# Kernel optimization log

Hardware: AMD Instinct MI355X
Metric: run time of the kernel (lower is better)

Reference implementation:

```python
import jax, jax.numpy as jnp
import numpy as np

H, DH = 8, 64          # num_heads, head_dim
DM = H * DH            # hidden_dim = 512
LAM = 1.0              # lambda_param
SCALE = 1.0 / np.sqrt(DH)


def setup_inputs() -> dict:
    key = jax.random.key(0)
    ks = jax.random.split(key, 12)
    B, N, R = 2, 2048, 16
    s = DM ** -0.5
    inp = {
        "x": jax.random.normal(ks[0], (B, N, DM), jnp.float32),
        "pde_residuals": jax.random.normal(ks[1], (B, N, R), jnp.float32),
        "mask": jnp.ones((B, 1, N, N), jnp.int32),
        "Wq": jax.random.normal(ks[2], (DM, DM), jnp.float32) * s,
        "bq": jax.random.normal(ks[3], (DM,), jnp.float32) * 0.01,
        "Wk": jax.random.normal(ks[4], (DM, DM), jnp.float32) * s,
        "bk": jax.random.normal(ks[5], (DM,), jnp.float32) * 0.01,
        "Wv": jax.random.normal(ks[6], (DM, DM), jnp.float32) * s,
        "bv": jax.random.normal(ks[7], (DM,), jnp.float32) * 0.01,
        "Wo": jax.random.normal(ks[8], (DM, DM), jnp.float32) * s,
        "bo": jax.random.normal(ks[9], (DM,), jnp.float32) * 0.01,
    }
    return inp


def reference(x, pde_residuals, mask, Wq, bq, Wk, bk, Wv, bv, Wo, bo):
    B, N, _ = x.shape
    # torch nn.Linear: y = x @ W.T + b
    q = (x @ Wq.T + bq).reshape(B, N, H, DH)
    k = (x @ Wk.T + bk).reshape(B, N, H, DH)
    v = (x @ Wv.T + bv).reshape(B, N, H, DH)
    # [B,H,N,N]
    scores = jnp.einsum('bqhd,bkhd->bhqk', q, k) * SCALE
    # residual bias: rb.unsqueeze(1) - rb.unsqueeze(2) -> bias[b,i,j] = rb[b,j] - rb[b,i]
    rb = jnp.linalg.norm(pde_residuals, axis=-1)            # [B,N]
    bias = rb[:, None, None, :] - rb[:, None, :, None]       # [B,1,N,N]
    scores = scores - LAM * bias
    scores = jnp.where(mask == 0, -jnp.inf, scores)
    attn = jax.nn.softmax(scores, axis=-1)                   # dropout is identity in eval
    out = jnp.einsum('bhqk,bkhd->bqhd', attn, v).reshape(B, N, DM)
    return out @ Wo.T + bo
```

## Files before the change

kernel.cpp:

```cpp
#include <hip/hip_runtime.h>
#include <hip/hip_bf16.h>
#include <math.h>

#define B_ 2
#define N_ 2048
#define H_ 8
#define DH_ 64
#define DM_ 512
#define R_ 16
#define LAM_ 1.0f
#define SCALE_ 0.125f
#define LOG2E_ 1.44269504088896f
#define QSCALE_ (SCALE_ * LOG2E_)
#define DEFER_THR_ 11.5415603f

typedef unsigned short u16;
typedef unsigned int u32;
typedef u16 u16x4 __attribute__((ext_vector_type(4)));
typedef u16 u16x8 __attribute__((ext_vector_type(8)));
typedef __bf16 bf16x8 __attribute__((ext_vector_type(8)));
typedef float f32x4 __attribute__((ext_vector_type(4)));

#define EXP2(x) __builtin_amdgcn_exp2f(x)

static __device__ __forceinline__ u16 f2bf(float f) {
    union { float f; unsigned u; } v; v.f = f;
    unsigned r = v.u + 0x7FFF + ((v.u >> 16) & 1);
    return (u16)(r >> 16);
}

static __device__ __forceinline__ u32 pack_bf16(float lo, float hi) {
    float2 f2; f2.x = lo; f2.y = hi;
    __hip_bfloat162 h2 = __float22bfloat162_rn(f2);
    u32 r;
    __builtin_memcpy(&r, &h2, 4);
    return r;
}

static __device__ __forceinline__ void gl_lds16(const void* g, void* l) {
    __builtin_amdgcn_global_load_lds(
        (const __attribute__((address_space(1))) unsigned*)g,
        (__attribute__((address_space(3))) unsigned*)l, 16, 0, 0);
}

__global__ __launch_bounds__(256) void prep(
    const float* __restrict__ x, const float* __restrict__ wq,
    const float* __restrict__ wk, const float* __restrict__ wv,
    const float* __restrict__ wo, u16* __restrict__ xb, u16* __restrict__ wqb,
    u16* __restrict__ wkb, u16* __restrict__ wvb, u16* __restrict__ wob) {
    int y = blockIdx.y;
    const float* src; u16* dst; int n;
    switch (y) {
        case 0: src = x;  dst = xb;  n = 2097152; break;
        case 1: src = wq; dst = wqb; n = 262144;  break;
        case 2: src = wk; dst = wkb; n = 262144;  break;
        case 3: src = wv; dst = wvb; n = 262144;  break;
        default: src = wo; dst = wob; n = 262144; break;
    }
    int i = (blockIdx.x * 256 + threadIdx.x) * 8;
    if (i >= n) return;
    float4 a = *(const float4*)(src + i);
    float4 b = *(const float4*)(src + i + 4);
    u16x8 o;
    o[0] = f2bf(a.x); o[1] = f2bf(a.y); o[2] = f2bf(a.z); o[3] = f2bf(a.w);
    o[4] = f2bf(b.x); o[5] = f2bf(b.y); o[6] = f2bf(b.z); o[7] = f2bf(b.w);
    *(u16x8*)(dst + i) = o;
}

struct Acc { f32x4 v[2][2]; };

static __device__ __forceinline__ Acc gemm_core(const u16* __restrict__ A,
                                                const u16* __restrict__ W,
                                                int m0, int nn0, char* LDSB) {
    int t = threadIdx.x, l = t & 63, w = t >> 6;
    int lg = l >> 4, li = l & 15;
    int wr = w >> 1, wc = w & 1;
    Acc acc;
#pragma unroll
    for (int m = 0; m < 2; ++m)
#pragma unroll
        for (int n = 0; n < 2; ++n) acc.v[m][n] = (f32x4){0.f, 0.f, 0.f, 0.f};

    int srl = l >> 3;
    int colb = ((l & 7) * 16) ^ (srl << 4);

    for (int k0 = 0; k0 < DM_; k0 += 64) {
        __syncthreads();
#pragma unroll
        for (int i = 0; i < 2; ++i) {
            int c = w * 2 + i;
            int row = c * 8 + srl;
            gl_lds16(A + (size_t)(m0 + row) * DM_ + k0 + (colb >> 1),
                     LDSB + c * 1024);
            gl_lds16(W + (size_t)(nn0 + row) * DM_ + k0 + (colb >> 1),
                     LDSB + 8192 + c * 1024);
        }
        __syncthreads();
#pragma unroll
        for (int kk = 0; kk < 2; ++kk) {
            bf16x8 af[2], bfr[2];
#pragma unroll
            for (int m = 0; m < 2; ++m) {
                int r = wr * 32 + m * 16 + li;
                af[m] = *(const bf16x8*)(LDSB + r * 128 +
                                         ((kk * 64 + lg * 16) ^ ((r & 7) << 4)));
            }
#pragma unroll
            for (int n = 0; n < 2; ++n) {
                int r = wc * 32 + n * 16 + li;
                bfr[n] = *(const bf16x8*)(LDSB + 8192 + r * 128 +
                                          ((kk * 64 + lg * 16) ^ ((r & 7) << 4)));
            }
#pragma unroll
            for (int m = 0; m < 2; ++m)
#pragma unroll
                for (int n = 0; n < 2; ++n)
                    acc.v[m][n] = __builtin_amdgcn_mfma_f32_16x16x32_bf16(
                        af[m], bfr[n], acc.v[m][n], 0, 0, 0);
        }
    }
    return acc;
}

struct Acc2 { f32x4 v[4][2]; };

static __device__ __forceinline__ Acc2 gemm_core2(const u16* __restrict__ A,
                                                  const u16* __restrict__ W,
                                                  int m0, int nn0, char* LDSB) {
    int t = threadIdx.x, l = t & 63, w = t >> 6;
    int lg = l >> 4, li = l & 15;
    int wr = w >> 1, wc = w & 1;
    Acc2 acc;
#pragma unroll
    for (int m = 0; m < 4; ++m)
#pragma unroll
        for (int n = 0; n < 2; ++n) acc.v[m][n] = (f32x4){0.f, 0.f, 0.f, 0.f};

    int srl = l >> 3;
    int colb = ((l & 7) * 16) ^ (srl << 4);

    for (int k0 = 0; k0 < DM_; k0 += 64) {
        __syncthreads();
#pragma unroll
        for (int i = 0; i < 4; ++i) {
            int c = w * 4 + i;
            int row = c * 8 + srl;
            gl_lds16(A + (size_t)(m0 + row) * DM_ + k0 + (colb >> 1),
                     LDSB + c * 1024);
        }
#pragma unroll
        for (int i = 0; i < 2; ++i) {
            int c = w * 2 + i;
            int row = c * 8 + srl;
            gl_lds16(W + (size_t)(nn0 + row) * DM_ + k0 + (colb >> 1),
                     LDSB + 16384 + c * 1024);
        }
        __syncthreads();
#pragma unroll
        for (int kk = 0; kk < 2; ++kk) {
            bf16x8 af[4], bfr[2];
#pragma unroll
            for (int m = 0; m < 4; ++m) {
                int r = wr * 64 + m * 16 + li;
                af[m] = *(const bf16x8*)(LDSB + r * 128 +
                                         ((kk * 64 + lg * 16) ^ ((r & 7) << 4)));
            }
#pragma unroll
            for (int n = 0; n < 2; ++n) {
                int r = wc * 32 + n * 16 + li;
                bfr[n] = *(const bf16x8*)(LDSB + 16384 + r * 128 +
                                          ((kk * 64 + lg * 16) ^ ((r & 7) << 4)));
            }
#pragma unroll
            for (int m = 0; m < 4; ++m)
#pragma unroll
                for (int n = 0; n < 2; ++n)
                    acc.v[m][n] = __builtin_amdgcn_mfma_f32_16x16x32_bf16(
                        af[m], bfr[n], acc.v[m][n], 0, 0, 0);
        }
    }
    return acc;
}

__global__ __launch_bounds__(256) void qkv_fused(
    const u16* __restrict__ xb, const u16* __restrict__ wqb,
    const u16* __restrict__ wkb, const u16* __restrict__ wvb,
    const float* __restrict__ bq, const float* __restrict__ bk,
    const float* __restrict__ bv, const int* __restrict__ mask,
    const float* __restrict__ pde, u16* __restrict__ q_bf,
    u16* __restrict__ k_bf, u16* __restrict__ vt,
    float* __restrict__ rbs, int* __restrict__ flags) {
    __shared__ char LDSB[24576];
    int bid = blockIdx.x, t = threadIdx.x;

    if (bid < 768) {
        int y = bid >> 5;
        int which = y >> 3;
        int nn0 = (y & 7) * 64;
        const u16* W = which == 0 ? wqb : which == 1 ? wkb : wvb;
        const float* bias = which == 0 ? bq : which == 1 ? bk : bv;
        int m0 = (bid & 31) * 128;
        Acc2 acc = gemm_core2(xb, W, m0, nn0, LDSB);

        int l = t & 63, w = t >> 6;
        int lg = l >> 4, li = l & 15;
        int wr = w >> 1, wc = w & 1;
        float scale = which == 0 ? QSCALE_ : 1.0f;
#pragma unroll
        for (int n = 0; n < 2; ++n) {
            int col = nn0 + wc * 32 + n * 16 + li;
            float bv_ = bias[col];
            if (which < 2) {
                u16* dst = which == 0 ? q_bf : k_bf;
#pragma unroll
                for (int m = 0; m < 4; ++m)
#pragma unroll
                    for (int r = 0; r < 4; ++r) {
                        int row = m0 + wr * 64 + m * 16 + lg * 4 + r;
                        dst[(size_t)row * DM_ + col] =
                            f2bf((acc.v[m][n][r] + bv_) * scale);
                    }
            } else {
                int h = col >> 6, d = col & 63;
#pragma unroll
                for (int m = 0; m < 4; ++m) {
                    int row = m0 + wr * 64 + m * 16 + lg * 4;
                    int b = row >> 11, nb = row & (N_ - 1);
                    u16x4 o;
#pragma unroll
                    for (int r = 0; r < 4; ++r) o[r] = f2bf(acc.v[m][n][r] + bv_);
                    *(u16x4*)(vt + ((size_t)((b * 8 + h) * 64 + d)) * N_ + nb) = o;
                }
            }
        }
    } else if (bid < 2816) {
        int idx = bid - 768;
        int b = idx >> 10, qt = (idx >> 5) & 31, kt = idx & 31;
        int* red = (int*)LDSB;
        if (t == 0) *red = 0;
        __syncthreads();
        int any = 0;
        for (int c = t; c < 1024; c += 256) {
            int row = c >> 4, seg = c & 15;
            int4 m4 = *(const int4*)(mask + (size_t)b * N_ * N_ +
                                     (size_t)(qt * 64 + row) * N_ + kt * 64 + seg * 4);
            any |= (m4.x == 0) | (m4.y == 0) | (m4.z == 0) | (m4.w == 0);
        }
        if (__ballot(any)) {
            if ((t & 63) == 0) atomicOr(red, 1);
        }
        __syncthreads();
        if (t == 0) flags[(b * 32 + qt) * 32 + kt] = *red;
    } else {
        int i = (bid - 2816) * 256 + t;
        if (i >= B_ * N_) return;
        const float4* p = (const float4*)(pde + (size_t)i * R_);
        float s = 0.f;
#pragma unroll
        for (int j = 0; j < 4; ++j) {
            float4 v = p[j];
            s += v.x * v.x + v.y * v.y + v.z * v.z + v.w * v.w;
        }
        rbs[i] = LAM_ * LOG2E_ * sqrtf(s);
    }
}

__global__ __launch_bounds__(256) void gemm_out(
    const u16* __restrict__ aob, const u16* __restrict__ wob,
    const float* __restrict__ bo, float* __restrict__ out) {
    __shared__ char LDSB[24576];
    int nn0 = blockIdx.y * 64;
    int m0 = blockIdx.x * 64;
    Acc acc = gemm_core(aob, wob, m0, nn0, LDSB);

    int t = threadIdx.x, l = t & 63, w = t >> 6;
    int lg = l >> 4, li = l & 15;
    int wr = w >> 1, wc = w & 1;
#pragma unroll
    for (int n = 0; n < 2; ++n) {
        int col = nn0 + wc * 32 + n * 16 + li;
        float bv_ = bo[col];
#pragma unroll
        for (int m = 0; m < 2; ++m)
#pragma unroll
            for (int r = 0; r < 4; ++r) {
                int row = m0 + wr * 32 + m * 16 + lg * 4 + r;
                out[(size_t)row * DM_ + col] = acc.v[m][n][r] + bv_;
            }
    }
}

__global__ __launch_bounds__(512) void attn12(
    const u16* __restrict__ qb, const u16* __restrict__ kb,
    const u16* __restrict__ vtb, const float* __restrict__ rbs,
    const int* __restrict__ mask, const int* __restrict__ flags,
    u16* __restrict__ aob) {
    __shared__ char KVB[2][2][16384];
    __shared__ char PsB[8][2048];

    int t = threadIdx.x, l = t & 63, w = t >> 6;
    int g2 = w >> 2, wq = w & 3;
    int raw = blockIdx.x;
    int sid = (raw & 7) * 64 + (raw >> 3);
    int bh = sid >> 5, qg = sid & 31;
    int b = bh >> 3, h = bh & 7;
    int m0 = qg * 64 + wq * 16;
    int lg = l >> 4, li = l & 15;
    int k0base = g2 * 1024;

    int srl = l >> 3;
    int colb = ((l & 7) * 16) ^ (srl << 4);

    bf16x8 qa[2];
    {
        const u16* qrow = qb + (size_t)(b * N_ + m0 + li) * DM_ + h * DH_;
        qa[0] = __builtin_bit_cast(bf16x8, *(const u16x8*)(qrow + lg * 8));
        qa[1] = __builtin_bit_cast(bf16x8, *(const u16x8*)(qrow + 32 + lg * 8));
    }

    f32x4 o[4];
#pragma unroll
    for (int dt = 0; dt < 4; ++dt) o[dt] = (f32x4){0.f, 0.f, 0.f, 0.f};
    float mrun = -INFINITY, lrun = 0.f;

    auto STAGE = [&](int bufi, int k0s) {
        char* base = &KVB[g2][bufi][0];
#pragma unroll
        for (int c = 0; c < 2; ++c) {
            int chunk = wq * 2 + c;
            int row = chunk * 8 + srl;
            gl_lds16(kb + (size_t)(b * N_ + k0s + row) * DM_ + h * DH_ + (colb >> 1),
                     base + chunk * 1024);
            gl_lds16(vtb + ((size_t)(bh * DH_ + row)) * N_ + k0s + (colb >> 1),
                     base + 8192 + chunk * 1024);
        }
    };

    STAGE(0, k0base);
    __syncthreads();

    char* pwbase = &PsB[w][0] + li * 16 + ((lg & 1) << 3);
    int slot_lohi = (lg >> 1);

    int buf = 0;
    for (int tt = 0; tt < 16; ++tt) {
        int k0 = k0base + tt * 64;
        if (tt < 15) STAGE(buf ^ 1, k0 + 64);

        const char* Kb = &KVB[g2][buf][0];
        const char* Vb = &KVB[g2][buf][8192];
        int flag = flags[(b * 32 + qg) * 32 + (k0 >> 6)];

        f32x4 st[4];
        __builtin_amdgcn_s_setprio(1);
#pragma unroll
        for (int kt = 0; kt < 4; ++kt) {
            st[kt] = (f32x4){0.f, 0.f, 0.f, 0.f};
#pragma unroll
            for (int s = 0; s < 2; ++s) {
                int key = kt * 16 + li;
                bf16x8 kf = *(const bf16x8*)(Kb + key * 128 +
                                             ((s * 64 + lg * 16) ^ ((key & 7) << 4)));
                st[kt] = __builtin_amdgcn_mfma_f32_16x16x32_bf16(kf, qa[s], st[kt],
                                                                 0, 0, 0);
            }
        }
        __builtin_amdgcn_s_setprio(0);

#pragma unroll
        for (int kt = 0; kt < 4; ++kt) {
            float4 rb4 = *(const float4*)(rbs + b * N_ + k0 + kt * 16 + lg * 4);
            st[kt][0] -= rb4.x; st[kt][1] -= rb4.y;
            st[kt][2] -= rb4.z; st[kt][3] -= rb4.w;
        }
        if (flag) {
#pragma unroll
            for (int kt = 0; kt < 4; ++kt)
#pragma unroll
                for (int r = 0; r < 4; ++r) {
                    int rowg = m0 + li;
                    int keyg = k0 + kt * 16 + lg * 4 + r;
                    if (mask[(size_t)b * N_ * N_ + (size_t)rowg * N_ + keyg] == 0)
                        st[kt][r] = -INFINITY;
                }
        }

        float m0_ = fmaxf(fmaxf(st[0][0], st[0][1]), fmaxf(st[0][2], st[0][3]));
        float m1_ = fmaxf(fmaxf(st[1][0], st[1][1]), fmaxf(st[1][2], st[1][3]));
        float m2_ = fmaxf(fmaxf(st[2][0], st[2][1]), fmaxf(st[2][2], st[2][3]));
        float m3_ = fmaxf(fmaxf(st[3][0], st[3][1]), fmaxf(st[3][2], st[3][3]));
        float mymax = fmaxf(fmaxf(m0_, m1_), fmaxf(m2_, m3_));
        if (!__all(mymax - mrun <= DEFER_THR_)) {
            float pmax = mymax;
            pmax = fmaxf(pmax, __shfl_xor(pmax, 16));
            pmax = fmaxf(pmax, __shfl_xor(pmax, 32));
            float mnew = fmaxf(fmaxf(mrun, pmax), -3.0e38f);
            float corr = EXP2(mrun - mnew);
            mrun = mnew;
            lrun *= corr;
#pragma unroll
            for (int dt = 0; dt < 4; ++dt)
#pragma unroll
                for (int r = 0; r < 4; ++r) o[dt][r] *= corr;
        }

#pragma unroll
        for (int kt = 0; kt < 4; ++kt) {
            float p0 = EXP2(st[kt][0] - mrun);
            float p1 = EXP2(st[kt][1] - mrun);
            float p2 = EXP2(st[kt][2] - mrun);
            float p3 = EXP2(st[kt][3] - mrun);
            lrun += (p0 + p1) + (p2 + p3);
            uint2 pkw;
            pkw.x = pack_bf16(p0, p1);
            pkw.y = pack_bf16(p2, p3);
            int slot = (kt >> 1) * 4 + (kt & 1) * 2 + slot_lohi;
            *(uint2*)(pwbase + (slot << 8)) = pkw;
        }

        bf16x8 pf[2];
#pragma unroll
        for (int s = 0; s < 2; ++s)
            pf[s] = *(const bf16x8*)(&PsB[w][0] + ((s * 4 + lg) << 8) + li * 16);
        __builtin_amdgcn_s_setprio(1);
#pragma unroll
        for (int dt = 0; dt < 4; ++dt)
#pragma unroll
            for (int s = 0; s < 2; ++s) {
                int d = dt * 16 + li;
                bf16x8 vf = *(const bf16x8*)(Vb + d * 128 +
                                             ((s * 64 + lg * 16) ^ ((d & 7) << 4)));
                o[dt] = __builtin_amdgcn_mfma_f32_16x16x32_bf16(vf, pf[s], o[dt],
                                                                0, 0, 0);
            }
        __builtin_amdgcn_s_setprio(0);

        __syncthreads();
        buf ^= 1;
    }

    lrun += __shfl_xor(lrun, 16);
    lrun += __shfl_xor(lrun, 32);

    float* cmb = (float*)&KVB[0][0][0];
    float* mlc = (float*)&PsB[0][0];
    if (g2 == 1) {
        float* dst = cmb + wq * 1088;
#pragma unroll
        for (int dt = 0; dt < 4; ++dt)
            *(f32x4*)(dst + li * 68 + dt * 16 + lg * 4) = o[dt];
        if (lg == 0) {
            float2 ml; ml.x = mrun; ml.y = lrun;
            *(float2*)(mlc + (wq * 16 + li) * 2) = ml;
        }
    }
    __syncthreads();
    if (g2 == 0) {
        float2 ml1 = *(const float2*)(mlc + (wq * 16 + li) * 2);
        float m = fmaxf(mrun, ml1.x);
        float w0 = EXP2(mrun - m), w1 = EXP2(ml1.x - m);
        float denom = 1.f / (lrun * w0 + ml1.y * w1);
        w0 *= denom; w1 *= denom;
        const float* src = cmb + wq * 1088;
        u16* orow = aob + (size_t)(b * N_ + m0 + li) * DM_ + h * DH_;
#pragma unroll
        for (int dt = 0; dt < 4; ++dt) {
            f32x4 p1 = *(const f32x4*)(src + li * 68 + dt * 16 + lg * 4);
            u16x4 ov;
#pragma unroll
            for (int r = 0; r < 4; ++r)
                ov[r] = f2bf(o[dt][r] * w0 + p1[r] * w1);
            *(u16x4*)(orow + dt * 16 + lg * 4) = ov;
        }
    }
}

extern "C" void kernel_launch(void* const* d_in, const int* in_sizes, int n_in,
                              void* d_out, int out_size, void* d_ws, size_t ws_size,
                              hipStream_t stream) {
    const float* x   = (const float*)d_in[0];
    const float* pde = (const float*)d_in[1];
    const int*   msk = (const int*)d_in[2];
    const float* Wq  = (const float*)d_in[3];
    const float* bq  = (const float*)d_in[4];
    const float* Wk  = (const float*)d_in[5];
    const float* bk  = (const float*)d_in[6];
    const float* Wv  = (const float*)d_in[7];
    const float* bv  = (const float*)d_in[8];
    const float* Wo  = (const float*)d_in[9];
    const float* bo  = (const float*)d_in[10];
    float* out = (float*)d_out;

    const size_t MAT = (size_t)B_ * N_ * DM_;
    const size_t WSZ = (size_t)DM_ * DM_;
    u16* xb   = (u16*)d_ws;
    u16* q_bf = xb + MAT;
    u16* k_bf = q_bf + MAT;
    u16* vt   = k_bf + MAT;
    u16* aob  = vt + MAT;
    u16* wqb  = aob + MAT;
    u16* wkb  = wqb + WSZ;
    u16* wvb  = wkb + WSZ;
    u16* wob  = wvb + WSZ;
    float* rbs = (float*)(wob + WSZ);
    int* flags = (int*)(rbs + B_ * N_);

    prep<<<dim3(1024, 5), 256, 0, stream>>>(x, Wq, Wk, Wv, Wo,
                                            xb, wqb, wkb, wvb, wob);

    qkv_fused<<<2832, 256, 0, stream>>>(xb, wqb, wkb, wvb, bq, bk, bv,
                                        msk, pde, q_bf, k_bf, vt, rbs, flags);

    attn12<<<512, 512, 0, stream>>>(q_bf, k_bf, vt, rbs, msk, flags, aob);

    gemm_out<<<dim3(64, 8), 256, 0, stream>>>(aob, wob, bo, out);
}
```

Baseline: 67.69 us.

## Switch attention to 32x32x16 MFMA with 32-row query tiles per wave

Rewrites the attention kernel so each wave handles 32 query rows with 32x32x16 bf16 MFMAs instead of 16 rows with 16x16x32. The block drops from 8 to 4 waves, and each wave stages twice as many K/V chunks. The P tile layout is reworked into a swizzled per-row buffer. The goal is fewer LDS fragment reads per FLOP and better MFMA efficiency. The cost is higher register pressure from the 16-wide accumulators and less latency hiding with fewer waves per block.

```diff
diff --git a/kernel.cpp b/kernel.cpp
--- a/kernel.cpp
+++ b/kernel.cpp
@@ -20,6 +20,7 @@
 typedef u16 u16x8 __attribute__((ext_vector_type(8)));
 typedef __bf16 bf16x8 __attribute__((ext_vector_type(8)));
 typedef float f32x4 __attribute__((ext_vector_type(4)));
+typedef float f32x16 __attribute__((ext_vector_type(16)));
 
 #define EXP2(x) __builtin_amdgcn_exp2f(x)
 
@@ -290,44 +291,49 @@
     }
 }
 
-__global__ __launch_bounds__(512) void attn12(
+__global__ __launch_bounds__(256) void attn13(
     const u16* __restrict__ qb, const u16* __restrict__ kb,
     const u16* __restrict__ vtb, const float* __restrict__ rbs,
     const int* __restrict__ mask, const int* __restrict__ flags,
     u16* __restrict__ aob) {
     __shared__ char KVB[2][2][16384];
-    __shared__ char PsB[8][2048];
+    __shared__ char PsB[4][4096];
 
     int t = threadIdx.x, l = t & 63, w = t >> 6;
-    int g2 = w >> 2, wq = w & 3;
+    int qh = w >> 1, ks = w & 1;
     int raw = blockIdx.x;
     int sid = (raw & 7) * 64 + (raw >> 3);
     int bh = sid >> 5, qg = sid & 31;
     int b = bh >> 3, h = bh & 7;
-    int m0 = qg * 64 + wq * 16;
-    int lg = l >> 4, li = l & 15;
-    int k0base = g2 * 1024;
+    int m0 = qg * 64 + qh * 32;
+    int q5 = l & 31, hi = l >> 5;
+    int k0base = ks * 1024;
 
     int srl = l >> 3;
     int colb = ((l & 7) * 16) ^ (srl << 4);
-
-    bf16x8 qa[2];
+    int q7s = (q5 & 7) << 4;
+
+    bf16x8 qa[4];
     {
-        const u16* qrow = qb + (size_t)(b * N_ + m0 + li) * DM_ + h * DH_;
-        qa[0] = __builtin_bit_cast(bf16x8, *(const u16x8*)(qrow + lg * 8));
-        qa[1] = __builtin_bit_cast(bf16x8, *(const u16x8*)(qrow + 32 + lg * 8));
-    }
-
-    f32x4 o[4];
-#pragma unroll
-    for (int dt = 0; dt < 4; ++dt) o[dt] = (f32x4){0.f, 0.f, 0.f, 0.f};
+        const u16* qrow = qb + (size_t)(b * N_ + m0 + q5) * DM_ + h * DH_;
+#pragma unroll
+        for (int s = 0; s < 4; ++s)
+            qa[s] = __builtin_bit_cast(bf16x8,
+                        *(const u16x8*)(qrow + s * 16 + hi * 8));
+    }
+
+    f32x16 o[2];
+#pragma unroll
+    for (int db = 0; db < 2; ++db)
+#pragma unroll
+        for (int r = 0; r < 16; ++r) o[db][r] = 0.f;
     float mrun = -INFINITY, lrun = 0.f;
 
     auto STAGE = [&](int bufi, int k0s) {
-        char* base = &KVB[g2][bufi][0];
-#pragma unroll
-        for (int c = 0; c < 2; ++c) {
-            int chunk = wq * 2 + c;
+        char* base = &KVB[ks][bufi][0];
+#pragma unroll
+        for (int c = 0; c < 4; ++c) {
+            int chunk = qh * 4 + c;
             int row = chunk * 8 + srl;
             gl_lds16(kb + (size_t)(b * N_ + k0s + row) * DM_ + h * DH_ + (colb >> 1),
                      base + chunk * 1024);
@@ -339,139 +345,146 @@
     STAGE(0, k0base);
     __syncthreads();
 
-    char* pwbase = &PsB[w][0] + li * 16 + ((lg & 1) << 3);
-    int slot_lohi = (lg >> 1);
+    char* prow = &PsB[w][0] + q5 * 128;
 
     int buf = 0;
     for (int tt = 0; tt < 16; ++tt) {
         int k0 = k0base + tt * 64;
         if (tt < 15) STAGE(buf ^ 1, k0 + 64);
 
-        const char* Kb = &KVB[g2][buf][0];
-        const char* Vb = &KVB[g2][buf][8192];
+        const char* Kb = &KVB[ks][buf][0];
+        const char* Vb = &KVB[ks][buf][8192];
         int flag = flags[(b * 32 + qg) * 32 + (k0 >> 6)];
 
-        f32x4 st[4];
+        f32x16 st[2];
         __builtin_amdgcn_s_setprio(1);
 #pragma unroll
-        for (int kt = 0; kt < 4; ++kt) {
-            st[kt] = (f32x4){0.f, 0.f, 0.f, 0.f};
-#pragma unroll
-            for (int s = 0; s < 2; ++s) {
-                int key = kt * 16 + li;
-                bf16x8 kf = *(const bf16x8*)(Kb + key * 128 +
-                                             ((s * 64 + lg * 16) ^ ((key & 7) << 4)));
-                st[kt] = __builtin_amdgcn_mfma_f32_16x16x32_bf16(kf, qa[s], st[kt],
-                                                                 0, 0, 0);
+        for (int kb2 = 0; kb2 < 2; ++kb2) {
+#pragma unroll
+            for (int r = 0; r < 16; ++r) st[kb2][r] = 0.f;
+#pragma unroll
+            for (int s = 0; s < 4; ++s) {
+                bf16x8 kf = *(const bf16x8*)(Kb + (kb2 * 32 + q5) * 128 +
+                                             ((s * 32 + hi * 16) ^ q7s));
+                st[kb2] = __builtin_amdgcn_mfma_f32_32x32x16_bf16(
+                    kf, qa[s], st[kb2], 0, 0, 0);
             }
         }
         __builtin_amdgcn_s_setprio(0);
 
 #pragma unroll
-        for (int kt = 0; kt < 4; ++kt) {
-            float4 rb4 = *(const float4*)(rbs + b * N_ + k0 + kt * 16 + lg * 4);
-            st[kt][0] -= rb4.x; st[kt][1] -= rb4.y;
-            st[kt][2] -= rb4.z; st[kt][3] -= rb4.w;
-        }
+        for (int kb2 = 0; kb2 < 2; ++kb2)
+#pragma unroll
+            for (int g = 0; g < 4; ++g) {
+                float4 rb4 = *(const float4*)(rbs + b * N_ + k0 + kb2 * 32 +
+                                              8 * g + 4 * hi);
+                st[kb2][4 * g + 0] -= rb4.x;
+                st[kb2][4 * g + 1] -= rb4.y;
+                st[kb2][4 * g + 2] -= rb4.z;
+                st[kb2][4 * g + 3] -= rb4.w;
+            }
         if (flag) {
 #pragma unroll
-            for (int kt = 0; kt < 4; ++kt)
-#pragma unroll
-                for (int r = 0; r < 4; ++r) {
-                    int rowg = m0 + li;
-                    int keyg = k0 + kt * 16 + lg * 4 + r;
+            for (int kb2 = 0; kb2 < 2; ++kb2)
+#pragma unroll
+                for (int r = 0; r < 16; ++r) {
+                    int keyg = k0 + kb2 * 32 + (r & 3) + 8 * (r >> 2) + 4 * hi;
+                    int rowg = m0 + q5;
                     if (mask[(size_t)b * N_ * N_ + (size_t)rowg * N_ + keyg] == 0)
-                        st[kt][r] = -INFINITY;
+                        st[kb2][r] = -INFINITY;
                 }
         }
 
-        float m0_ = fmaxf(fmaxf(st[0][0], st[0][1]), fmaxf(st[0][2], st[0][3]));
-        float m1_ = fmaxf(fmaxf(st[1][0], st[1][1]), fmaxf(st[1][2], st[1][3]));
-        float m2_ = fmaxf(fmaxf(st[2][0], st[2][1]), fmaxf(st[2][2], st[2][3]));
-        float m3_ = fmaxf(fmaxf(st[3][0], st[3][1]), fmaxf(st[3][2], st[3][3]));
-        float mymax = fmaxf(fmaxf(m0_, m1_), fmaxf(m2_, m3_));
+        float mymax = -INFINITY;
+#pragma unroll
+        for (int kb2 = 0; kb2 < 2; ++kb2)
+#pragma unroll
+            for (int r = 0; r < 16; ++r) mymax = fmaxf(mymax, st[kb2][r]);
         if (!__all(mymax - mrun <= DEFER_THR_)) {
-            float pmax = mymax;
-            pmax = fmaxf(pmax, __shfl_xor(pmax, 16));
-            pmax = fmaxf(pmax, __shfl_xor(pmax, 32));
+            float pmax = fmaxf(mymax, __shfl_xor(mymax, 32));
             float mnew = fmaxf(fmaxf(mrun, pmax), -3.0e38f);
             float corr = EXP2(mrun - mnew);
             mrun = mnew;
             lrun *= corr;
 #pragma unroll
-            for (int dt = 0; dt < 4; ++dt)
-#pragma unroll
-                for (int r = 0; r < 4; ++r) o[dt][r] *= corr;
-        }
-
-#pragma unroll
-        for (int kt = 0; kt < 4; ++kt) {
-            float p0 = EXP2(st[kt][0] - mrun);
-            float p1 = EXP2(st[kt][1] - mrun);
-            float p2 = EXP2(st[kt][2] - mrun);
-            float p3 = EXP2(st[kt][3] - mrun);
-            lrun += (p0 + p1) + (p2 + p3);
-            uint2 pkw;
-            pkw.x = pack_bf16(p0, p1);
-            pkw.y = pack_bf16(p2, p3);
-            int slot = (kt >> 1) * 4 + (kt & 1) * 2 + slot_lohi;
-            *(uint2*)(pwbase + (slot << 8)) = pkw;
-        }
-
-        bf16x8 pf[2];
-#pragma unroll
-        for (int s = 0; s < 2; ++s)
-            pf[s] = *(const bf16x8*)(&PsB[w][0] + ((s * 4 + lg) << 8) + li * 16);
+            for (int db = 0; db < 2; ++db)
+#pragma unroll
+                for (int r = 0; r < 16; ++r) o[db][r] *= corr;
+        }
+
+#pragma unroll
+        for (int kb2 = 0; kb2 < 2; ++kb2)
+#pragma unroll
+            for (int g = 0; g < 4; ++g) {
+                float p0 = EXP2(st[kb2][4 * g + 0] - mrun);
+                float p1 = EXP2(st[kb2][4 * g + 1] - mrun);
+                float p2 = EXP2(st[kb2][4 * g + 2] - mrun);
+                float p3 = EXP2(st[kb2][4 * g + 3] - mrun);
+                lrun += (p0 + p1) + (p2 + p3);
+                uint2 pkw;
+                pkw.x = pack_bf16(p0, p1);
+                pkw.y = pack_bf16(p2, p3);
+                *(uint2*)(prow + ((kb2 * 64 + 16 * g + 8 * hi) ^ q7s)) = pkw;
+            }
+
         __builtin_amdgcn_s_setprio(1);
 #pragma unroll
-        for (int dt = 0; dt < 4; ++dt)
-#pragma unroll
-            for (int s = 0; s < 2; ++s) {
-                int d = dt * 16 + li;
-                bf16x8 vf = *(const bf16x8*)(Vb + d * 128 +
-                                             ((s * 64 + lg * 16) ^ ((d & 7) << 4)));
-                o[dt] = __builtin_amdgcn_mfma_f32_16x16x32_bf16(vf, pf[s], o[dt],
-                                                                0, 0, 0);
-            }
+        for (int ks16 = 0; ks16 < 4; ++ks16) {
+            bf16x8 pf = *(const bf16x8*)(prow + ((ks16 * 32 + hi * 16) ^ q7s));
+#pragma unroll
+            for (int db = 0; db < 2; ++db) {
+                bf16x8 vf = *(const bf16x8*)(Vb + (db * 32 + q5) * 128 +
+                                             ((ks16 * 32 + hi * 16) ^ q7s));
+                o[db] = __builtin_amdgcn_mfma_f32_32x32x16_bf16(
+                    vf, pf, o[db], 0, 0, 0);
+            }
+        }
         __builtin_amdgcn_s_setprio(0);
 
         __syncthreads();
         buf ^= 1;
     }
 
-    lrun += __shfl_xor(lrun, 16);
     lrun += __shfl_xor(lrun, 32);
 
     float* cmb = (float*)&KVB[0][0][0];
     float* mlc = (float*)&PsB[0][0];
-    if (g2 == 1) {
-        float* dst = cmb + wq * 1088;
-#pragma unroll
-        for (int dt = 0; dt < 4; ++dt)
-            *(f32x4*)(dst + li * 68 + dt * 16 + lg * 4) = o[dt];
-        if (lg == 0) {
+    if (ks == 1) {
+        float* dst = cmb + qh * 2176 + q5 * 68;
+#pragma unroll
+        for (int db = 0; db < 2; ++db)
+#pragma unroll
+            for (int g = 0; g < 4; ++g) {
+                f32x4 v4;
+                v4[0] = o[db][4 * g + 0]; v4[1] = o[db][4 * g + 1];
+                v4[2] = o[db][4 * g + 2]; v4[3] = o[db][4 * g + 3];
+                *(f32x4*)(dst + db * 32 + 8 * g + 4 * hi) = v4;
+            }
+        if (hi == 0) {
             float2 ml; ml.x = mrun; ml.y = lrun;
-            *(float2*)(mlc + (wq * 16 + li) * 2) = ml;
+            *(float2*)(mlc + (qh * 32 + q5) * 2) = ml;
         }
     }
     __syncthreads();
-    if (g2 == 0) {
-        float2 ml1 = *(const float2*)(mlc + (wq * 16 + li) * 2);
+    if (ks == 0) {
+        float2 ml1 = *(const float2*)(mlc + (qh * 32 + q5) * 2);
         float m = fmaxf(mrun, ml1.x);
         float w0 = EXP2(mrun - m), w1 = EXP2(ml1.x - m);
         float denom = 1.f / (lrun * w0 + ml1.y * w1);
         w0 *= denom; w1 *= denom;
-        const float* src = cmb + wq * 1088;
-        u16* orow = aob + (size_t)(b * N_ + m0 + li) * DM_ + h * DH_;
-#pragma unroll
-        for (int dt = 0; dt < 4; ++dt) {
-            f32x4 p1 = *(const f32x4*)(src + li * 68 + dt * 16 + lg * 4);
-            u16x4 ov;
-#pragma unroll
-            for (int r = 0; r < 4; ++r)
-                ov[r] = f2bf(o[dt][r] * w0 + p1[r] * w1);
-            *(u16x4*)(orow + dt * 16 + lg * 4) = ov;
-        }
+        const float* src = cmb + qh * 2176 + q5 * 68;
+        u16* orow = aob + (size_t)(b * N_ + m0 + q5) * DM_ + h * DH_;
+#pragma unroll
+        for (int db = 0; db < 2; ++db)
+#pragma unroll
+            for (int g = 0; g < 4; ++g) {
+                f32x4 p1 = *(const f32x4*)(src + db * 32 + 8 * g + 4 * hi);
+                u16x4 ov;
+#pragma unroll
+                for (int m4 = 0; m4 < 4; ++m4)
+                    ov[m4] = f2bf(o[db][4 * g + m4] * w0 + p1[m4] * w1);
+                *(u16x4*)(orow + db * 32 + 8 * g + 4 * hi) = ov;
+            }
     }
 }
 
@@ -511,7 +524,7 @@
     qkv_fused<<<2832, 256, 0, stream>>>(xb, wqb, wkb, wvb, bq, bk, bv,
                                         msk, pde, q_bf, k_bf, vt, rbs, flags);
 
-    attn12<<<512, 512, 0, stream>>>(q_bf, k_bf, vt, rbs, msk, flags, aob);
+    attn13<<<512, 256, 0, stream>>>(q_bf, k_bf, vt, rbs, msk, flags, aob);
 
     gemm_out<<<dim3(64, 8), 256, 0, stream>>>(aob, wob, bo, out);
 }
```

Result: slower. 71.45 us (+5.6%).
